# Performance work log

Hardware: AMD Instinct MI355X
Metric: run time of the kernel (lower is better)

## Reference

```python
import jax, jax.numpy as jnp
import numpy as np

BLOCK_SIZE = 128
N_EMBD = 600
HEAD_SIZE = 75
BATCH = 512


def setup_inputs() -> dict:
    key = jax.random.key(0)
    kx, kq, kk, kv = jax.random.split(key, 4)
    x = jax.random.normal(kx, (BATCH, BLOCK_SIZE, N_EMBD), dtype=jnp.float32)
    # nn.Linear(n_embd, head_size, bias=False); store as [in, out] so y = x @ W
    s = 1.0 / np.sqrt(N_EMBD)
    Wq = jax.random.uniform(kq, (N_EMBD, HEAD_SIZE), jnp.float32, -s, s)
    Wk = jax.random.uniform(kk, (N_EMBD, HEAD_SIZE), jnp.float32, -s, s)
    Wv = jax.random.uniform(kv, (N_EMBD, HEAD_SIZE), jnp.float32, -s, s)
    return {"x": x, "Wq": Wq, "Wk": Wk, "Wv": Wv}


def reference(x, Wq, Wk, Wv):
    B, T, C = x.shape
    q = jnp.einsum("btc,ch->bth", x, Wq)
    k = jnp.einsum("btc,ch->bth", x, Wk)
    v = jnp.einsum("btc,ch->bth", x, Wv)
    # NOTE: source scales by C**-0.5 with C = n_embd (not head_size)
    scale = jnp.asarray(C, x.dtype) ** -0.5
    wei = jnp.einsum("bth,bsh->bts", q, k) * scale  # [B, T, T]
    causal = jnp.tril(jnp.ones((T, T), dtype=bool))
    wei = jnp.where(causal, wei, -jnp.inf)
    attn = jax.nn.softmax(wei, axis=-1)
    # dropout is identity in eval/reference mode
    return jnp.einsum("bts,bsh->bth", attn, v)
```

## Files before the change

kernel.cpp:

```cpp
#include <hip/hip_runtime.h>
#include <stdint.h>
#include <math.h>

#define TT 128
#define CC 600
#define HH 75

typedef __attribute__((ext_vector_type(8)))  short bh8;
typedef __attribute__((ext_vector_type(16))) float f32x16;
typedef __attribute__((ext_vector_type(4)))  float f32x4;

#define XA_OFF 0
#define P_OFF  0
#define PM_OFF 16384
#define PS_OFF 17408
#define Q_OFF  20480
#define K_OFF  40960
#define V_OFF  61440
#define LDS_BYTES 81920

__device__ __forceinline__ uint32_t f2bf1(float f) {
  uint32_t u = __float_as_uint(f);
  return (u + 0x7FFFu + ((u >> 16) & 1u)) >> 16;
}
__device__ __forceinline__ uint32_t packbf(float a, float b) {
  return f2bf1(a) | (f2bf1(b) << 16);
}
__device__ __forceinline__ float bfrt(float f) {
  return __uint_as_float(f2bf1(f) << 16);
}
__device__ __forceinline__ int swz(int row, int bytein) {
  return row * 256 + (bytein ^ ((row & 7) << 4));
}
__device__ __forceinline__ int pswz(int row, int bytein) {
  return row * 128 + (bytein ^ ((row & 7) << 4));
}

__global__ void pack_w_kernel(const float* __restrict__ Wq, const float* __restrict__ Wk,
                              const float* __restrict__ Wv, uint16_t* __restrict__ wpack) {
  const int cs  = blockIdx.x;
  const int tid = threadIdx.x;
  const int n   = tid >> 1;
  const int h5  = tid & 1;
  const int sec = n / 80;
  const int h   = n - sec * 80;
  const float* W = (sec == 0) ? Wq : (sec == 1) ? Wk : (sec == 2) ? Wv : nullptr;
  const bool valid = (W != nullptr) && (h < HH);
  const int k0 = cs * 16 + h5 * 8;
  uint32_t u[4] = {0u, 0u, 0u, 0u};
  if (valid) {
#pragma unroll
    for (int j = 0; j < 8; ++j) {
      const int k = k0 + j;
      float v = (k < CC) ? W[k * HH + h] : 0.f;
      u[j >> 1] |= f2bf1(v) << ((j & 1) * 16);
    }
  }
  ((uint4*)wpack)[cs * 512 + n * 2 + h5] = make_uint4(u[0], u[1], u[2], u[3]);
}

__global__ __launch_bounds__(512, 4) void head_kernel(
    const float* __restrict__ x, const uint16_t* __restrict__ wpack,
    float* __restrict__ out)
{
  __shared__ char smem[LDS_BYTES];
  const int tid  = threadIdx.x;
  const int b    = blockIdx.x;
  const int lane = tid & 63;
  const int wv   = tid >> 6;
  const int l31  = lane & 31;
  const int h5   = lane >> 5;

  const int m0 = (wv >> 2) * 64;
  const int n0 = (wv & 3) * 64;

  f32x16 acc[2][2];
#pragma unroll
  for (int mi = 0; mi < 2; ++mi)
#pragma unroll
    for (int ni = 0; ni < 2; ++ni)
#pragma unroll
      for (int r = 0; r < 16; ++r) acc[mi][ni][r] = 0.f;

  const int xt  = tid >> 2;
  const int xcg = tid & 3;
  const float* xrow = x + (size_t)b * (TT * CC) + (size_t)xt * CC;
  const bh8* wfp = (const bh8*)wpack;
  const int woff = (n0 + l31) * 2 + h5;

  {
    float4 p0 = *(const float4*)(xrow + xcg * 4);
    float4 p1 = *(const float4*)(xrow + 16 + xcg * 4);
    char* xa = smem + XA_OFF;
    *(uint2*)(xa + xt * 80 + xcg * 8)      = make_uint2(packbf(p0.x, p0.y), packbf(p0.z, p0.w));
    *(uint2*)(xa + xt * 80 + 32 + xcg * 8) = make_uint2(packbf(p1.x, p1.y), packbf(p1.z, p1.w));
    __syncthreads();
  }

  for (int c = 0; c < 19; ++c) {
    const int  buf  = c & 1;
    const bool more = (c + 1 < 19);
    bh8 w00 = wfp[(c * 2 + 0) * 512 + 0  + woff];
    bh8 w01 = wfp[(c * 2 + 0) * 512 + 64 + woff];
    bh8 w10 = wfp[(c * 2 + 1) * 512 + 0  + woff];
    bh8 w11 = wfp[(c * 2 + 1) * 512 + 64 + woff];
    float4 p0, p1;
    if (more) {
      const int cc = c + 1;
      p0 = *(const float4*)(xrow + cc * 32 + xcg * 4);
      const int c2 = cc * 32 + 16 + xcg * 4;
      p1 = *(const float4*)(xrow + ((c2 < CC) ? c2 : 0));
    }
    const char* xa = smem + XA_OFF + buf * 10240;
#pragma unroll
    for (int ks = 0; ks < 2; ++ks) {
      bh8 af[2];
#pragma unroll
      for (int mi = 0; mi < 2; ++mi)
        af[mi] = *(const bh8*)(xa + (m0 + mi * 32 + l31) * 80 + ks * 32 + h5 * 16);
      const bh8 b0 = ks ? w10 : w00;
      const bh8 b1 = ks ? w11 : w01;
#pragma unroll
      for (int mi = 0; mi < 2; ++mi) {
        acc[mi][0] = __builtin_amdgcn_mfma_f32_32x32x16_bf16(af[mi], b0, acc[mi][0], 0, 0, 0);
        acc[mi][1] = __builtin_amdgcn_mfma_f32_32x32x16_bf16(af[mi], b1, acc[mi][1], 0, 0, 0);
      }
    }
    if (more) {
      const int nb = buf ^ 1;
      char* xaw = smem + XA_OFF + nb * 10240;
      *(uint2*)(xaw + xt * 80 + xcg * 8)      = make_uint2(packbf(p0.x, p0.y), packbf(p0.z, p0.w));
      *(uint2*)(xaw + xt * 80 + 32 + xcg * 8) = make_uint2(packbf(p1.x, p1.y), packbf(p1.z, p1.w));
    }
    __syncthreads();
  }

#pragma unroll
  for (int mi = 0; mi < 2; ++mi) {
    const int tb = m0 + mi * 32;
#pragma unroll
    for (int ni = 0; ni < 2; ++ni) {
      const int nn = n0 + ni * 32 + l31;
      if (nn < 160) {
        const int h = (nn < 80) ? nn : nn - 80;
        char* base = smem + ((nn < 80) ? Q_OFF : K_OFF) + (h >> 4) * 4096 + (h & 15) * 2;
#pragma unroll
        for (int r = 0; r < 16; ++r) {
          const int t = tb + (r & 3) + 8 * (r >> 2) + 4 * h5;
          *(uint16_t*)(base + t * 32) = (uint16_t)f2bf1(acc[mi][ni][r]);
        }
      } else if (nn < 240) {
        const int hh2 = nn - 160;
#pragma unroll
        for (int g = 0; g < 4; ++g) {
          const int t0 = tb + 8 * g + 4 * h5;
          *(uint2*)(smem + V_OFF + swz(hh2, t0 * 2)) =
            make_uint2(packbf(acc[mi][ni][4*g],   acc[mi][ni][4*g+1]),
                       packbf(acc[mi][ni][4*g+2], acc[mi][ni][4*g+3]));
        }
      }
    }
  }
  __syncthreads();

  const int mt2 = wv & 1;
  const int tq  = (wv >> 1) * 32 + l31;
  f32x16 sac[2];
#pragma unroll
  for (int ts2 = 0; ts2 < 2; ++ts2)
#pragma unroll
    for (int r = 0; r < 16; ++r) sac[ts2][r] = 0.f;

#pragma unroll
  for (int ks = 0; ks < 5; ++ks) {
    const bh8 qf = *(const bh8*)(smem + Q_OFF + ks * 4096 + tq * 32 + h5 * 16);
#pragma unroll
    for (int ts2 = 0; ts2 < 2; ++ts2) {
      const int sr = (mt2 * 2 + ts2) * 32 + l31;
      const bh8 kf = *(const bh8*)(smem + K_OFF + ks * 4096 + sr * 32 + h5 * 16);
      sac[ts2] = __builtin_amdgcn_mfma_f32_32x32x16_bf16(kf, qf, sac[ts2], 0, 0, 0);
    }
  }

  float pvv[32];
  float vmax = -INFINITY;
  const float scl = 0.040824829046386302f;
#pragma unroll
  for (int ts2 = 0; ts2 < 2; ++ts2) {
    const int st = (mt2 * 2 + ts2) * 32;
#pragma unroll
    for (int r = 0; r < 16; ++r) {
      const int s = st + (r & 3) + 8 * (r >> 2) + 4 * h5;
      float v = sac[ts2][r] * scl;
      v = (s <= tq) ? v : -INFINITY;
      pvv[ts2 * 16 + r] = v;
      vmax = fmaxf(vmax, v);
    }
  }
  vmax = fmaxf(vmax, __shfl_xor(vmax, 32));
  float* pmb = (float*)(smem + PM_OFF);
  float* psb = (float*)(smem + PS_OFF);
  if (h5 == 0) pmb[mt2 * 128 + tq] = vmax;
  __syncthreads();
  const float mrow = fmaxf(pmb[tq], pmb[128 + tq]);
  float sum = 0.f;
#pragma unroll
  for (int i = 0; i < 32; ++i) {
    const float p = bfrt(__expf(pvv[i] - mrow));
    pvv[i] = p;
    sum += p;
  }
  sum += __shfl_xor(sum, 32);
  if (h5 == 0) psb[mt2 * 128 + tq] = sum;
  if (mt2 == 0) {
#pragma unroll
    for (int ts2 = 0; ts2 < 2; ++ts2) {
#pragma unroll
      for (int g = 0; g < 4; ++g) {
        const int sl = ts2 * 32 + 8 * g + 4 * h5;
        *(uint2*)(smem + P_OFF + pswz(tq, sl * 2)) =
          make_uint2(packbf(pvv[ts2*16+4*g],   pvv[ts2*16+4*g+1]),
                     packbf(pvv[ts2*16+4*g+2], pvv[ts2*16+4*g+3]));
      }
    }
  }
  __syncthreads();

  const int l15   = lane & 15;
  const int q4    = lane >> 4;
  const int trow0 = wv * 16;
  f32x4 oac[5];
#pragma unroll
  for (int nt = 0; nt < 5; ++nt)
#pragma unroll
    for (int r = 0; r < 4; ++r) oac[nt][r] = 0.f;

#pragma unroll
  for (int ksl = 0; ksl < 2; ++ksl) {
    const int kb = ksl * 64 + q4 * 16;
    const bh8 pf = *(const bh8*)(smem + P_OFF + pswz(trow0 + l15, kb));
#pragma unroll
    for (int nt = 0; nt < 5; ++nt) {
      const bh8 vf = *(const bh8*)(smem + V_OFF + swz(nt * 16 + l15, kb));
      oac[nt] = __builtin_amdgcn_mfma_f32_16x16x32_bf16(pf, vf, oac[nt], 0, 0, 0);
    }
  }
  __syncthreads();
  if (mt2 == 1) {
#pragma unroll
    for (int ts2 = 0; ts2 < 2; ++ts2) {
#pragma unroll
      for (int g = 0; g < 4; ++g) {
        const int sl = ts2 * 32 + 8 * g + 4 * h5;
        *(uint2*)(smem + P_OFF + pswz(tq, sl * 2)) =
          make_uint2(packbf(pvv[ts2*16+4*g],   pvv[ts2*16+4*g+1]),
                     packbf(pvv[ts2*16+4*g+2], pvv[ts2*16+4*g+3]));
      }
    }
  }
  __syncthreads();
#pragma unroll
  for (int ksl = 0; ksl < 2; ++ksl) {
    const int kb = ksl * 64 + q4 * 16;
    const bh8 pf = *(const bh8*)(smem + P_OFF + pswz(trow0 + l15, kb));
#pragma unroll
    for (int nt = 0; nt < 5; ++nt) {
      const bh8 vf = *(const bh8*)(smem + V_OFF + swz(nt * 16 + l15, 128 + kb));
      oac[nt] = __builtin_amdgcn_mfma_f32_16x16x32_bf16(pf, vf, oac[nt], 0, 0, 0);
    }
  }

  const float* psf = (const float*)(smem + PS_OFF);
  float rinv[4];
#pragma unroll
  for (int r = 0; r < 4; ++r) {
    const int t = trow0 + q4 * 4 + r;
    rinv[r] = 1.0f / (psf[t] + psf[128 + t]);
  }
  float* ob = out + (size_t)b * (TT * HH);
#pragma unroll
  for (int nt = 0; nt < 5; ++nt) {
    const int h = nt * 16 + l15;
    if (h < HH) {
#pragma unroll
      for (int r = 0; r < 4; ++r) {
        const int t = trow0 + q4 * 4 + r;
        ob[t * HH + h] = oac[nt][r] * rinv[r];
      }
    }
  }
}

extern "C" void kernel_launch(void* const* d_in, const int* in_sizes, int n_in,
                              void* d_out, int out_size, void* d_ws, size_t ws_size,
                              hipStream_t stream) {
  (void)in_sizes; (void)n_in; (void)out_size; (void)ws_size;
  const float* x  = (const float*)d_in[0];
  const float* Wq = (const float*)d_in[1];
  const float* Wk = (const float*)d_in[2];
  const float* Wv = (const float*)d_in[3];
  uint16_t* wpack = (uint16_t*)d_ws;
  float* out = (float*)d_out;
  pack_w_kernel<<<38, 512, 0, stream>>>(Wq, Wk, Wv, wpack);
  head_kernel<<<512, 512, 0, stream>>>(x, wpack, out);
}
```

Before: 249.8 us.

## Stage x via direct global-to-LDS loads and spill V to global workspace

Loads fp32 x tiles straight into LDS with global_load_lds (XOR-swizzled, double-buffered) and converts them to bf16 when building MFMA fragments, instead of staging through registers with bf16 packing on store. To fit the fp32 tiles in LDS, the V projection is written to a per-block global workspace and read back from global (through cache) during the PV matmul, with a threadfence added. This removes the register round trip for x but doubles LDS traffic for x, repeats the conversion per fragment read, and adds global memory latency on V reads.

```diff
diff --git a/kernel.cpp b/kernel.cpp
--- a/kernel.cpp
+++ b/kernel.cpp
@@ -1,4 +1,5 @@
 #include <hip/hip_runtime.h>
+#include <hip/hip_bf16.h>
 #include <stdint.h>
 #include <math.h>
 
@@ -14,10 +15,11 @@
 #define P_OFF  0
 #define PM_OFF 16384
 #define PS_OFF 17408
-#define Q_OFF  20480
-#define K_OFF  40960
-#define V_OFF  61440
-#define LDS_BYTES 81920
+#define Q_OFF  32768
+#define K_OFF  53248
+#define LDS_BYTES 73728
+
+#define VWS_OFF 524288
 
 __device__ __forceinline__ uint32_t f2bf1(float f) {
   uint32_t u = __float_as_uint(f);
@@ -29,11 +31,13 @@
 __device__ __forceinline__ float bfrt(float f) {
   return __uint_as_float(f2bf1(f) << 16);
 }
-__device__ __forceinline__ int swz(int row, int bytein) {
-  return row * 256 + (bytein ^ ((row & 7) << 4));
-}
 __device__ __forceinline__ int pswz(int row, int bytein) {
   return row * 128 + (bytein ^ ((row & 7) << 4));
+}
+__device__ __forceinline__ void gl_lds16(const float* g, char* l) {
+  __builtin_amdgcn_global_load_lds(
+      (const __attribute__((address_space(1))) unsigned int*)(const void*)g,
+      (__attribute__((address_space(3))) unsigned int*)l, 16, 0, 0);
 }
 
 __global__ void pack_w_kernel(const float* __restrict__ Wq, const float* __restrict__ Wk,
@@ -61,7 +65,7 @@
 
 __global__ __launch_bounds__(512, 4) void head_kernel(
     const float* __restrict__ x, const uint16_t* __restrict__ wpack,
-    float* __restrict__ out)
+    uint16_t* __restrict__ vws, float* __restrict__ out)
 {
   __shared__ char smem[LDS_BYTES];
   const int tid  = threadIdx.x;
@@ -82,42 +86,53 @@
 #pragma unroll
       for (int r = 0; r < 16; ++r) acc[mi][ni][r] = 0.f;
 
-  const int xt  = tid >> 2;
-  const int xcg = tid & 3;
-  const float* xrow = x + (size_t)b * (TT * CC) + (size_t)xt * CC;
+  const int sxt  = tid >> 3;
+  const int sxs  = (tid & 7) ^ (sxt & 7);
+  const float* xrow0 = x + (size_t)b * (TT * CC) + (size_t)sxt * CC;
+  const float* xrow1 = xrow0 + (size_t)64 * CC;
+  char* const ld0 = smem + XA_OFF + tid * 16;
   const bh8* wfp = (const bh8*)wpack;
   const int woff = (n0 + l31) * 2 + h5;
+  uint16_t* vtb = vws + (size_t)b * (80 * 128);
 
   {
-    float4 p0 = *(const float4*)(xrow + xcg * 4);
-    float4 p1 = *(const float4*)(xrow + 16 + xcg * 4);
-    char* xa = smem + XA_OFF;
-    *(uint2*)(xa + xt * 80 + xcg * 8)      = make_uint2(packbf(p0.x, p0.y), packbf(p0.z, p0.w));
-    *(uint2*)(xa + xt * 80 + 32 + xcg * 8) = make_uint2(packbf(p1.x, p1.y), packbf(p1.z, p1.w));
+    const int kc = sxs * 4;
+    gl_lds16(xrow0 + kc, ld0);
+    gl_lds16(xrow1 + kc, ld0 + 8192);
     __syncthreads();
   }
 
   for (int c = 0; c < 19; ++c) {
-    const int  buf  = c & 1;
-    const bool more = (c + 1 < 19);
+    const int buf = c & 1;
+    if (c + 1 < 19) {
+      int kc = (c + 1) * 32 + sxs * 4;
+      if (kc >= CC) kc = 0;
+      char* ldn = ld0 + (buf ^ 1) * 16384;
+      gl_lds16(xrow0 + kc, ldn);
+      gl_lds16(xrow1 + kc, ldn + 8192);
+    }
     bh8 w00 = wfp[(c * 2 + 0) * 512 + 0  + woff];
     bh8 w01 = wfp[(c * 2 + 0) * 512 + 64 + woff];
     bh8 w10 = wfp[(c * 2 + 1) * 512 + 0  + woff];
     bh8 w11 = wfp[(c * 2 + 1) * 512 + 64 + woff];
-    float4 p0, p1;
-    if (more) {
-      const int cc = c + 1;
-      p0 = *(const float4*)(xrow + cc * 32 + xcg * 4);
-      const int c2 = cc * 32 + 16 + xcg * 4;
-      p1 = *(const float4*)(xrow + ((c2 < CC) ? c2 : 0));
-    }
-    const char* xa = smem + XA_OFF + buf * 10240;
+    const char* xa = smem + XA_OFF + buf * 16384;
 #pragma unroll
     for (int ks = 0; ks < 2; ++ks) {
       bh8 af[2];
 #pragma unroll
-      for (int mi = 0; mi < 2; ++mi)
-        af[mi] = *(const bh8*)(xa + (m0 + mi * 32 + l31) * 80 + ks * 32 + h5 * 16);
+      for (int mi = 0; mi < 2; ++mi) {
+        const int t = m0 + mi * 32 + l31;
+        const int s0 = (ks * 4 + h5 * 2) ^ (t & 7);
+        const int s1 = (ks * 4 + h5 * 2 + 1) ^ (t & 7);
+        const float4 fa = *(const float4*)(xa + t * 128 + s0 * 16);
+        const float4 fb = *(const float4*)(xa + t * 128 + s1 * 16);
+        union { bh8 v; __hip_bfloat162 h[4]; } u;
+        u.h[0] = __float22bfloat162_rn(make_float2(fa.x, fa.y));
+        u.h[1] = __float22bfloat162_rn(make_float2(fa.z, fa.w));
+        u.h[2] = __float22bfloat162_rn(make_float2(fb.x, fb.y));
+        u.h[3] = __float22bfloat162_rn(make_float2(fb.z, fb.w));
+        af[mi] = u.v;
+      }
       const bh8 b0 = ks ? w10 : w00;
       const bh8 b1 = ks ? w11 : w01;
 #pragma unroll
@@ -125,12 +140,6 @@
         acc[mi][0] = __builtin_amdgcn_mfma_f32_32x32x16_bf16(af[mi], b0, acc[mi][0], 0, 0, 0);
         acc[mi][1] = __builtin_amdgcn_mfma_f32_32x32x16_bf16(af[mi], b1, acc[mi][1], 0, 0, 0);
       }
-    }
-    if (more) {
-      const int nb = buf ^ 1;
-      char* xaw = smem + XA_OFF + nb * 10240;
-      *(uint2*)(xaw + xt * 80 + xcg * 8)      = make_uint2(packbf(p0.x, p0.y), packbf(p0.z, p0.w));
-      *(uint2*)(xaw + xt * 80 + 32 + xcg * 8) = make_uint2(packbf(p1.x, p1.y), packbf(p1.z, p1.w));
     }
     __syncthreads();
   }
@@ -154,13 +163,14 @@
 #pragma unroll
         for (int g = 0; g < 4; ++g) {
           const int t0 = tb + 8 * g + 4 * h5;
-          *(uint2*)(smem + V_OFF + swz(hh2, t0 * 2)) =
+          *(uint2*)((char*)vtb + hh2 * 256 + t0 * 2) =
             make_uint2(packbf(acc[mi][ni][4*g],   acc[mi][ni][4*g+1]),
                        packbf(acc[mi][ni][4*g+2], acc[mi][ni][4*g+3]));
         }
       }
     }
   }
+  __threadfence();
   __syncthreads();
 
   const int mt2 = wv & 1;
@@ -241,7 +251,7 @@
     const bh8 pf = *(const bh8*)(smem + P_OFF + pswz(trow0 + l15, kb));
 #pragma unroll
     for (int nt = 0; nt < 5; ++nt) {
-      const bh8 vf = *(const bh8*)(smem + V_OFF + swz(nt * 16 + l15, kb));
+      const bh8 vf = *(const bh8*)((const char*)vtb + (nt * 16 + l15) * 256 + kb);
       oac[nt] = __builtin_amdgcn_mfma_f32_16x16x32_bf16(pf, vf, oac[nt], 0, 0, 0);
     }
   }
@@ -265,7 +275,7 @@
     const bh8 pf = *(const bh8*)(smem + P_OFF + pswz(trow0 + l15, kb));
 #pragma unroll
     for (int nt = 0; nt < 5; ++nt) {
-      const bh8 vf = *(const bh8*)(smem + V_OFF + swz(nt * 16 + l15, 128 + kb));
+      const bh8 vf = *(const bh8*)((const char*)vtb + (nt * 16 + l15) * 256 + 128 + kb);
       oac[nt] = __builtin_amdgcn_mfma_f32_16x16x32_bf16(pf, vf, oac[nt], 0, 0, 0);
     }
   }
@@ -300,7 +310,8 @@
   const float* Wk = (const float*)d_in[2];
   const float* Wv = (const float*)d_in[3];
   uint16_t* wpack = (uint16_t*)d_ws;
+  uint16_t* vws   = (uint16_t*)((char*)d_ws + VWS_OFF);
   float* out = (float*)d_out;
   pack_w_kernel<<<38, 512, 0, stream>>>(Wq, Wk, Wv, wpack);
-  head_kernel<<<512, 512, 0, stream>>>(x, wpack, out);
-}
+  head_kernel<<<512, 512, 0, stream>>>(x, wpack, vws, out);
+}
```

Result: slower. 409.7 us (+64.1%).
